# Optimization experiments

Measured on AMD Instinct MI355X. Metric: run time of the kernel, lower is better.

Reference implementation:

```python
import jax, jax.numpy as jnp
import numpy as np

B = 64          # decode batch (one token per sequence)
HID = 4096      # hidden_size
HQ = 32         # num query heads
HKV = 8         # num kv heads (GQA, groups = 4)
D = 128         # head_dim
BS = 16         # block_size of paged KV cache
MAXB = 64       # max blocks per sequence -> max context 1024
MAXPOS = 4096   # rope table length
TOTAL_SLOTS = B * MAXB * BS


def setup_inputs() -> dict:
    key = jax.random.key(0)
    ks = jax.random.split(key, 10)
    hidden = jax.random.normal(ks[0], (B, 1, HID), jnp.float32)
    context_lens = jax.random.randint(ks[1], (B,), 512, BS * MAXB + 1).astype(jnp.int32)
    positions = (context_lens - 1).reshape(B, 1)  # decoding token position
    # each sequence owns a contiguous range of blocks
    block_tables = jnp.arange(B * MAXB, dtype=jnp.int32).reshape(B, MAXB)
    last = context_lens - 1
    slot_mapping = (block_tables[jnp.arange(B), last // BS] * BS + last % BS).astype(jnp.int32)
    inv_freq = 1.0 / (10000.0 ** (jnp.arange(0, D, 2, dtype=jnp.float32) / D))
    freqs = jnp.outer(jnp.arange(MAXPOS, dtype=jnp.float32), inv_freq)  # [MAXPOS, D/2]
    cos, sin = jnp.cos(freqs), jnp.sin(freqs)
    key_cache = jax.random.normal(ks[2], (TOTAL_SLOTS, HKV, D), jnp.float32) * 0.5
    value_cache = jax.random.normal(ks[3], (TOTAL_SLOTS, HKV, D), jnp.float32) * 0.5
    Wq = jax.random.normal(ks[4], (HQ * D, HID), jnp.float32) * 0.02
    Wk = jax.random.normal(ks[5], (HKV * D, HID), jnp.float32) * 0.02
    Wv = jax.random.normal(ks[6], (HKV * D, HID), jnp.float32) * 0.02
    Wo = jax.random.normal(ks[7], (HID, HQ * D), jnp.float32) * 0.02
    return dict(hidden=hidden, positions=positions, cos=cos, sin=sin,
                key_cache=key_cache, value_cache=value_cache,
                slot_mapping=slot_mapping, block_tables=block_tables,
                context_lens=context_lens, Wq=Wq, Wk=Wk, Wv=Wv, Wo=Wo)


def reference(hidden, positions, cos, sin, key_cache, value_cache,
              slot_mapping, block_tables, context_lens, Wq, Wk, Wv, Wo):
    b, s, _ = hidden.shape  # s == 1 (paged decode path)
    q = (hidden @ Wq.T).reshape(b, s, HQ, D)
    k = (hidden @ Wk.T).reshape(b, s, HKV, D)
    v = (hidden @ Wv.T).reshape(b, s, HKV, D)
    # rotary embedding (half-split convention)
    c = cos[positions][:, :, None, :]  # [b,s,1,D/2]
    sn = sin[positions][:, :, None, :]
    def rope(x):
        x1, x2 = jnp.split(x, 2, axis=-1)
        return jnp.concatenate([x1 * c - x2 * sn, x2 * c + x1 * sn], axis=-1)
    q, k = rope(q), rope(k)
    # scatter current token's K/V into the paged cache via slot_mapping
    kc = key_cache.at[slot_mapping].set(k.reshape(-1, HKV, D))
    vc = value_cache.at[slot_mapping].set(v.reshape(-1, HKV, D))
    # gather each sequence's KV via block tables
    T = MAXB * BS
    t = jnp.arange(T)
    slots = block_tables[:, t // BS] * BS + (t % BS)  # [b, T]
    keys = kc[slots]   # [b, T, HKV, D]
    vals = vc[slots]   # [b, T, HKV, D]
    # GQA attention, q has one token per sequence
    G = HQ // HKV
    qg = q.reshape(b, HKV, G, D)
    scores = jnp.einsum('bkgd,btkd->bkgt', qg, keys) / jnp.sqrt(jnp.float32(D))
    mask = t[None, :] < context_lens[:, None]  # [b, T]
    scores = jnp.where(mask[:, None, None, :], scores, -jnp.inf)
    p = jax.nn.softmax(scores, axis=-1)
    out = jnp.einsum('bkgt,btkd->bkgd', p, vals).reshape(b, 1, HQ * D)
    return out @ Wo.T
```

## Files before the change

### kernel.cpp

```cpp
#include <hip/hip_runtime.h>

#define B_    64
#define HID_  4096
#define HQ_   32
#define HKV_  8
#define D_    128
#define BS_   16
#define MAXB_ 64

#define KSPLIT  16
#define KCHUNK  (HID_ / KSPLIT)
#define QKV_ROWS 6144
#define O_ROWS   4096
#define SPLITS  8

#define REGION_SZ ((size_t)KSPLIT * QKV_ROWS * 64)
#define QKVF_SZ  ((size_t)64 * 6144)
#define ATTN_SZ  ((size_t)64 * 4096)
#define XB_SZ    ((size_t)HID_ * 64)

typedef __attribute__((ext_vector_type(8))) short bf16x8;
typedef __attribute__((ext_vector_type(4))) float f32x4;

__device__ inline unsigned short f2bf(float x) {
  union { float f; unsigned u; } v; v.f = x;
  unsigned r = v.u + 0x7fff + ((v.u >> 16) & 1);
  return (unsigned short)(r >> 16);
}
__device__ inline float bf2f(unsigned short h) {
  union { float f; unsigned u; } v; v.u = ((unsigned)h) << 16; return v.f;
}

__global__ __launch_bounds__(256) void convert_x(
    const float* __restrict__ X, unsigned short* __restrict__ XBhi,
    unsigned short* __restrict__ XBlo)
{
  int idx = blockIdx.x * 256 + threadIdx.x;
  int kg = idx >> 6, b = idx & 63;
  const float* xp = X + (size_t)b * HID_ + kg * 8;
  float4 a = *(const float4*)xp, c = *(const float4*)(xp + 4);
  float xs[8] = {a.x, a.y, a.z, a.w, c.x, c.y, c.z, c.w};
  unsigned short hi[8], lo[8];
  #pragma unroll
  for (int j = 0; j < 8; ++j) {
    hi[j] = f2bf(xs[j]);
    lo[j] = f2bf(xs[j] - bf2f(hi[j]));
  }
  *(uint4*)(XBhi + (size_t)idx * 8) = *(const uint4*)hi;
  *(uint4*)(XBlo + (size_t)idx * 8) = *(const uint4*)lo;
}

__global__ __launch_bounds__(256, 4) void gemm_mfma(
    const float* __restrict__ W0, const float* __restrict__ W1,
    const float* __restrict__ W2,
    const unsigned short* __restrict__ XBhi,
    const unsigned short* __restrict__ XBlo,
    int split1, int split2, int rows_total, float* __restrict__ part)
{
  const int tid = threadIdx.x;
  const int l   = tid & 63;
  const int w   = tid >> 6;
  const int r0  = blockIdx.x * 128 + w * 32;
  const int k0  = blockIdx.y * KCHUNK;

  const float* W; int rloc;
  if (r0 < split1)      { W = W0; rloc = r0; }
  else if (r0 < split2) { W = W1; rloc = r0 - split1; }
  else                  { W = W2; rloc = r0 - split2; }

  const int lm = l & 15;
  const int lk = l >> 4;

  const float* wp0 = W + (size_t)(rloc + lm) * HID_ + k0 + lk * 8;
  const float* wp1 = wp0 + (size_t)16 * HID_;
  const unsigned short* bh = XBhi + ((size_t)(k0 / 8 + lk) * 64 + lm) * 8;
  const unsigned short* bl = XBlo + ((size_t)(k0 / 8 + lk) * 64 + lm) * 8;

  f32x4 acc[2][4];
  #pragma unroll
  for (int rt = 0; rt < 2; ++rt)
    #pragma unroll
    for (int ct = 0; ct < 4; ++ct)
      #pragma unroll
      for (int i = 0; i < 4; ++i) acc[rt][ct][i] = 0.f;

  #pragma unroll 2
  for (int ks = 0; ks < KCHUNK / 32; ++ks) {
    bf16x8 Bh[4], Bl[4];
    #pragma unroll
    for (int ct = 0; ct < 4; ++ct) {
      Bh[ct] = *(const bf16x8*)(bh + (size_t)ks * 2048 + ct * 128);
      Bl[ct] = *(const bf16x8*)(bl + (size_t)ks * 2048 + ct * 128);
    }
    #pragma unroll
    for (int rt = 0; rt < 2; ++rt) {
      const float* wp = (rt ? wp1 : wp0) + ks * 32;
      float4 a0 = *(const float4*)wp;
      float4 a1 = *(const float4*)(wp + 4);
      float xs[8] = {a0.x, a0.y, a0.z, a0.w, a1.x, a1.y, a1.z, a1.w};
      bf16x8 Ah, Al;
      #pragma unroll
      for (int j = 0; j < 8; ++j) {
        unsigned short h = f2bf(xs[j]);
        Ah[j] = (short)h;
        Al[j] = (short)f2bf(xs[j] - bf2f(h));
      }
      #pragma unroll
      for (int ct = 0; ct < 4; ++ct) {
        acc[rt][ct] = __builtin_amdgcn_mfma_f32_16x16x32_bf16(Ah, Bh[ct], acc[rt][ct], 0, 0, 0);
        acc[rt][ct] = __builtin_amdgcn_mfma_f32_16x16x32_bf16(Al, Bh[ct], acc[rt][ct], 0, 0, 0);
        acc[rt][ct] = __builtin_amdgcn_mfma_f32_16x16x32_bf16(Ah, Bl[ct], acc[rt][ct], 0, 0, 0);
      }
    }
  }

  #pragma unroll
  for (int rt = 0; rt < 2; ++rt)
    #pragma unroll
    for (int ct = 0; ct < 4; ++ct) {
      int row = r0 + rt * 16 + lk * 4;
      int bat = ct * 16 + lm;
      #pragma unroll
      for (int i = 0; i < 4; ++i)
        part[((size_t)blockIdx.y * rows_total + row + i) * 64 + bat] = acc[rt][ct][i];
    }
}

__global__ __launch_bounds__(256) void reduce_rope(
    const float* __restrict__ part, const float* __restrict__ cosT,
    const float* __restrict__ sinT, const int* __restrict__ positions,
    float* __restrict__ qkvf)
{
  const int bb  = threadIdx.x & 63;
  const int cid = blockIdx.x * 4 + (threadIdx.x >> 6);
  const int pos = positions[bb];

  if (cid < 2048) {
    const int hq = cid >> 6, d0 = cid & 63;
    const int r1 = hq * 128 + d0;
    float x1 = 0.f, x2 = 0.f;
    #pragma unroll 8
    for (int ks = 0; ks < KSPLIT; ++ks) {
      x1 += part[((size_t)ks * QKV_ROWS + r1) * 64 + bb];
      x2 += part[((size_t)ks * QKV_ROWS + r1 + 64) * 64 + bb];
    }
    float c = cosT[pos * 64 + d0], s = sinT[pos * 64 + d0];
    const float scale = 0.08838834764831843f;
    qkvf[(size_t)(bb * 32 + hq) * 128 + d0]      = (x1 * c - x2 * s) * scale;
    qkvf[(size_t)(bb * 32 + hq) * 128 + d0 + 64] = (x2 * c + x1 * s) * scale;
  } else if (cid < 2560) {
    const int c2 = cid - 2048;
    const int kh = c2 >> 6, d0 = c2 & 63;
    const int r1 = 4096 + kh * 128 + d0;
    float x1 = 0.f, x2 = 0.f;
    #pragma unroll 8
    for (int ks = 0; ks < KSPLIT; ++ks) {
      x1 += part[((size_t)ks * QKV_ROWS + r1) * 64 + bb];
      x2 += part[((size_t)ks * QKV_ROWS + r1 + 64) * 64 + bb];
    }
    float c = cosT[pos * 64 + d0], s = sinT[pos * 64 + d0];
    qkvf[262144 + (size_t)(bb * 8 + kh) * 128 + d0]      = x1 * c - x2 * s;
    qkvf[262144 + (size_t)(bb * 8 + kh) * 128 + d0 + 64] = x2 * c + x1 * s;
  } else {
    const int c2 = cid - 2560;
    const int kh = c2 >> 6, d0 = c2 & 63;
    const int r1 = 5120 + kh * 128 + d0;
    float x1 = 0.f, x2 = 0.f;
    #pragma unroll 8
    for (int ks = 0; ks < KSPLIT; ++ks) {
      x1 += part[((size_t)ks * QKV_ROWS + r1) * 64 + bb];
      x2 += part[((size_t)ks * QKV_ROWS + r1 + 64) * 64 + bb];
    }
    qkvf[327680 + (size_t)(bb * 8 + kh) * 128 + d0]      = x1;
    qkvf[327680 + (size_t)(bb * 8 + kh) * 128 + d0 + 64] = x2;
  }
}

__global__ __launch_bounds__(256) void attn_split(
    const float* __restrict__ qkvf, const float* __restrict__ kcache,
    const float* __restrict__ vcache, const int* __restrict__ btab,
    const int* __restrict__ ctxlen,
    float* __restrict__ part_o,
    float* __restrict__ part_ml)
{
  const int bid = blockIdx.x;
  const int s   = bid & (SPLITS - 1);
  const int bh  = bid >> 3;
  const int b = bh >> 3, h = bh & 7;
  const int ctx   = ctxlen[b];
  const int chunk = (ctx + SPLITS - 1) / SPLITS;
  const int t0 = s * chunk;
  const int t1 = min(ctx, t0 + chunk);
  const int n  = t1 - t0;
  const int last = ctx - 1;

  const int tid  = threadIdx.x;
  const int half = tid >> 5;
  const int d4   = tid & 31;

  __shared__ float sc[4][128];
  __shared__ float oacc[8][4][128];
  __shared__ float red[4][2];

  float4 qf[4];
  #pragma unroll
  for (int g = 0; g < 4; ++g)
    qf[g] = *(const float4*)(qkvf + (size_t)(b * 32 + h * 4 + g) * 128 + d4 * 4);

  const float* knew = qkvf + 262144 + (size_t)(b * 8 + h) * 128;
  const float* vnew = qkvf + 327680 + (size_t)(b * 8 + h) * 128;

  for (int t = t0 + half; t < t1; t += 8) {
    const float* kp;
    if (t == last) kp = knew;
    else {
      int slot = btab[b * MAXB_ + (t >> 4)] * BS_ + (t & 15);
      kp = kcache + ((size_t)slot * HKV_ + h) * D_;
    }
    float4 kv = *(const float4*)(kp + d4 * 4);
    float p0 = qf[0].x * kv.x + qf[0].y * kv.y + qf[0].z * kv.z + qf[0].w * kv.w;
    float p1 = qf[1].x * kv.x + qf[1].y * kv.y + qf[1].z * kv.z + qf[1].w * kv.w;
    float p2 = qf[2].x * kv.x + qf[2].y * kv.y + qf[2].z * kv.z + qf[2].w * kv.w;
    float p3 = qf[3].x * kv.x + qf[3].y * kv.y + qf[3].z * kv.z + qf[3].w * kv.w;
    #pragma unroll
    for (int m = 16; m >= 1; m >>= 1) {
      p0 += __shfl_xor(p0, m);
      p1 += __shfl_xor(p1, m);
      p2 += __shfl_xor(p2, m);
      p3 += __shfl_xor(p3, m);
    }
    if (d4 == 0) {
      int i = t - t0;
      sc[0][i] = p0; sc[1][i] = p1; sc[2][i] = p2; sc[3][i] = p3;
    }
  }
  __syncthreads();

  {
    const int w = tid >> 6, l = tid & 63;
    float mx = -1e30f;
    for (int i = l; i < n; i += 64) mx = fmaxf(mx, sc[w][i]);
    #pragma unroll
    for (int m = 32; m >= 1; m >>= 1) mx = fmaxf(mx, __shfl_xor(mx, m));
    float lsum = 0.f;
    for (int i = l; i < n; i += 64) {
      float p = __expf(sc[w][i] - mx);
      sc[w][i] = p;
      lsum += p;
    }
    #pragma unroll
    for (int m = 32; m >= 1; m >>= 1) lsum += __shfl_xor(lsum, m);
    if (l == 0) { red[w][0] = mx; red[w][1] = lsum; }
  }
  __syncthreads();

  float acc[4][4] = {{0.f}};
  for (int t = t0 + half; t < t1; t += 8) {
    const float* vp;
    if (t == last) vp = vnew;
    else {
      int slot = btab[b * MAXB_ + (t >> 4)] * BS_ + (t & 15);
      vp = vcache + ((size_t)slot * HKV_ + h) * D_;
    }
    float4 vv = *(const float4*)(vp + d4 * 4);
    int i = t - t0;
    #pragma unroll
    for (int g = 0; g < 4; ++g) {
      float p = sc[g][i];
      acc[g][0] += p * vv.x; acc[g][1] += p * vv.y;
      acc[g][2] += p * vv.z; acc[g][3] += p * vv.w;
    }
  }
  #pragma unroll
  for (int g = 0; g < 4; ++g)
    #pragma unroll
    for (int j = 0; j < 4; ++j)
      oacc[half][g][d4 * 4 + j] = acc[g][j];
  __syncthreads();

  for (int idx = tid; idx < 512; idx += 256) {
    int g = idx >> 7, d = idx & 127;
    float v = 0.f;
    #pragma unroll
    for (int hh = 0; hh < 8; ++hh) v += oacc[hh][g][d];
    part_o[(size_t)bid * 512 + idx] = v;
  }
  if (tid < 8) part_ml[(size_t)bid * 8 + tid] = red[tid >> 1][tid & 1];
}

__global__ __launch_bounds__(256) void attn_combine(
    const float* __restrict__ part_o, const float* __restrict__ part_ml,
    float* __restrict__ attn_out)
{
  const int bh = blockIdx.x;
  const int tid = threadIdx.x;

  __shared__ float Sg[SPLITS][4];
  __shared__ float Dg[4];

  if (tid < 32) {
    int s = tid >> 2, g = tid & 3;
    float m = part_ml[((size_t)bh * SPLITS + s) * 8 + g * 2];
    float l = part_ml[((size_t)bh * SPLITS + s) * 8 + g * 2 + 1];
    float M = m;
    #pragma unroll
    for (int k = 4; k <= 16; k <<= 1) M = fmaxf(M, __shfl_xor(M, k));
    float scl = __expf(m - M);
    float dl = l * scl;
    #pragma unroll
    for (int k = 4; k <= 16; k <<= 1) dl += __shfl_xor(dl, k);
    Sg[s][g] = scl;
    if (s == 0) Dg[g] = dl;
  }
  __syncthreads();

  for (int idx = tid; idx < 512; idx += 256) {
    int g = idx >> 7;
    float num = 0.f;
    #pragma unroll
    for (int s = 0; s < SPLITS; ++s)
      num += Sg[s][g] * part_o[((size_t)bh * SPLITS + s) * 512 + idx];
    attn_out[(size_t)bh * 512 + idx] = num / Dg[g];
  }
}

__global__ __launch_bounds__(256) void reduce_out_t(
    const float* __restrict__ part, float* __restrict__ out)
{
  __shared__ float t[64][65];
  const int i0 = blockIdx.x * 64;
  const int lane = threadIdx.x & 63, q = threadIdx.x >> 6;

  #pragma unroll
  for (int rr = q; rr < 64; rr += 4) {
    float s = 0.f;
    #pragma unroll 8
    for (int ks = 0; ks < KSPLIT; ++ks)
      s += part[((size_t)ks * O_ROWS + i0 + rr) * 64 + lane];
    t[rr][lane] = s;
  }
  __syncthreads();
  #pragma unroll
  for (int rr = q; rr < 64; rr += 4)
    out[(size_t)rr * O_ROWS + i0 + lane] = t[lane][rr];
}

extern "C" void kernel_launch(void* const* d_in, const int* in_sizes, int n_in,
                              void* d_out, int out_size, void* d_ws, size_t ws_size,
                              hipStream_t stream)
{
  (void)in_sizes; (void)n_in; (void)out_size; (void)ws_size;
  const float* hidden    = (const float*)d_in[0];
  const int*   positions = (const int*)d_in[1];
  const float* cosT      = (const float*)d_in[2];
  const float* sinT      = (const float*)d_in[3];
  const float* kcache    = (const float*)d_in[4];
  const float* vcache    = (const float*)d_in[5];
  const int*   btab      = (const int*)d_in[7];
  const int*   ctx       = (const int*)d_in[8];
  const float* Wq        = (const float*)d_in[9];
  const float* Wk        = (const float*)d_in[10];
  const float* Wv        = (const float*)d_in[11];
  const float* Wo        = (const float*)d_in[12];
  float* out = (float*)d_out;

  float* ws      = (float*)d_ws;
  float* region  = ws;
  float* qkvf    = region + REGION_SZ;
  float* attn_o  = qkvf + QKVF_SZ;
  unsigned short* XBhi = (unsigned short*)(attn_o + ATTN_SZ);
  unsigned short* XBlo = XBhi + XB_SZ;
  float* part1   = region;
  float* part_o  = region;
  float* part_ml = region + (size_t)B_ * HKV_ * SPLITS * 512;
  float* part3   = region;

  convert_x<<<128, 256, 0, stream>>>(hidden, XBhi, XBlo);
  gemm_mfma<<<dim3(QKV_ROWS / 128, KSPLIT), 256, 0, stream>>>(
      Wq, Wk, Wv, XBhi, XBlo, 4096, 5120, QKV_ROWS, part1);
  reduce_rope<<<768, 256, 0, stream>>>(part1, cosT, sinT, positions, qkvf);
  attn_split<<<B_ * HKV_ * SPLITS, 256, 0, stream>>>(
      qkvf, kcache, vcache, btab, ctx, part_o, part_ml);
  attn_combine<<<B_ * HKV_, 256, 0, stream>>>(part_o, part_ml, attn_o);
  convert_x<<<128, 256, 0, stream>>>(attn_o, XBhi, XBlo);
  gemm_mfma<<<dim3(O_ROWS / 128, KSPLIT), 256, 0, stream>>>(
      Wo, Wo, Wo, XBhi, XBlo, O_ROWS, O_ROWS, O_ROWS, part3);
  reduce_out_t<<<O_ROWS / 64, 256, 0, stream>>>(part3, out);
}
```

Baseline: 203.4 us.

## Fuse attention combine with bf16 split conversion, double K-split, shrink attn LDS

The attention-combine kernel now writes the hi/lo bf16 split layout directly, so the separate convert_x launch and the fp32 attention-output buffer are removed. The GEMM K-split is raised from 16 to 32 with a fully unrolled inner loop, which gives the grid more blocks but makes the reduction kernels read twice as many partials. The attn_split kernel does a cross-half shuffle reduction before writing to a smaller shared buffer, and declares a minimum-occupancy launch bound. Together these aim to cut launch overhead and traffic and raise parallelism, at the cost of more partial-sum memory traffic and a larger workspace region.

```diff
diff --git a/kernel.cpp b/kernel.cpp
--- a/kernel.cpp
+++ b/kernel.cpp
@@ -8,15 +8,15 @@
 #define BS_   16
 #define MAXB_ 64
 
-#define KSPLIT  16
-#define KCHUNK  (HID_ / KSPLIT)
+#define KS1     32
+#define KCHUNK  (HID_ / KS1)
+#define NSTEP   (KCHUNK / 32)
 #define QKV_ROWS 6144
 #define O_ROWS   4096
 #define SPLITS  8
 
-#define REGION_SZ ((size_t)KSPLIT * QKV_ROWS * 64)
+#define REGION_SZ ((size_t)KS1 * QKV_ROWS * 64)
 #define QKVF_SZ  ((size_t)64 * 6144)
-#define ATTN_SZ  ((size_t)64 * 4096)
 #define XB_SZ    ((size_t)HID_ * 64)
 
 typedef __attribute__((ext_vector_type(8))) short bf16x8;
@@ -84,8 +84,8 @@
       #pragma unroll
       for (int i = 0; i < 4; ++i) acc[rt][ct][i] = 0.f;
 
-  #pragma unroll 2
-  for (int ks = 0; ks < KCHUNK / 32; ++ks) {
+  #pragma unroll
+  for (int ks = 0; ks < NSTEP; ++ks) {
     bf16x8 Bh[4], Bl[4];
     #pragma unroll
     for (int ct = 0; ct < 4; ++ct) {
@@ -140,7 +140,7 @@
     const int r1 = hq * 128 + d0;
     float x1 = 0.f, x2 = 0.f;
     #pragma unroll 8
-    for (int ks = 0; ks < KSPLIT; ++ks) {
+    for (int ks = 0; ks < KS1; ++ks) {
       x1 += part[((size_t)ks * QKV_ROWS + r1) * 64 + bb];
       x2 += part[((size_t)ks * QKV_ROWS + r1 + 64) * 64 + bb];
     }
@@ -154,7 +154,7 @@
     const int r1 = 4096 + kh * 128 + d0;
     float x1 = 0.f, x2 = 0.f;
     #pragma unroll 8
-    for (int ks = 0; ks < KSPLIT; ++ks) {
+    for (int ks = 0; ks < KS1; ++ks) {
       x1 += part[((size_t)ks * QKV_ROWS + r1) * 64 + bb];
       x2 += part[((size_t)ks * QKV_ROWS + r1 + 64) * 64 + bb];
     }
@@ -167,7 +167,7 @@
     const int r1 = 5120 + kh * 128 + d0;
     float x1 = 0.f, x2 = 0.f;
     #pragma unroll 8
-    for (int ks = 0; ks < KSPLIT; ++ks) {
+    for (int ks = 0; ks < KS1; ++ks) {
       x1 += part[((size_t)ks * QKV_ROWS + r1) * 64 + bb];
       x2 += part[((size_t)ks * QKV_ROWS + r1 + 64) * 64 + bb];
     }
@@ -176,7 +176,7 @@
   }
 }
 
-__global__ __launch_bounds__(256) void attn_split(
+__global__ __launch_bounds__(256, 8) void attn_split(
     const float* __restrict__ qkvf, const float* __restrict__ kcache,
     const float* __restrict__ vcache, const int* __restrict__ btab,
     const int* __restrict__ ctxlen,
@@ -199,7 +199,7 @@
   const int d4   = tid & 31;
 
   __shared__ float sc[4][128];
-  __shared__ float oacc[8][4][128];
+  __shared__ float wred[4][4][128];
   __shared__ float red[4][2];
 
   float4 qf[4];
@@ -275,24 +275,31 @@
   for (int g = 0; g < 4; ++g)
     #pragma unroll
     for (int j = 0; j < 4; ++j)
-      oacc[half][g][d4 * 4 + j] = acc[g][j];
+      acc[g][j] += __shfl_xor(acc[g][j], 32);
+  if ((tid & 32) == 0) {
+    int wv = tid >> 6;
+    #pragma unroll
+    for (int g = 0; g < 4; ++g)
+      #pragma unroll
+      for (int j = 0; j < 4; ++j)
+        wred[wv][g][d4 * 4 + j] = acc[g][j];
+  }
   __syncthreads();
 
   for (int idx = tid; idx < 512; idx += 256) {
     int g = idx >> 7, d = idx & 127;
-    float v = 0.f;
-    #pragma unroll
-    for (int hh = 0; hh < 8; ++hh) v += oacc[hh][g][d];
+    float v = wred[0][g][d] + wred[1][g][d] + wred[2][g][d] + wred[3][g][d];
     part_o[(size_t)bid * 512 + idx] = v;
   }
   if (tid < 8) part_ml[(size_t)bid * 8 + tid] = red[tid >> 1][tid & 1];
 }
 
-__global__ __launch_bounds__(256) void attn_combine(
+__global__ __launch_bounds__(256) void attn_combine_xb(
     const float* __restrict__ part_o, const float* __restrict__ part_ml,
-    float* __restrict__ attn_out)
+    unsigned short* __restrict__ XBhi, unsigned short* __restrict__ XBlo)
 {
   const int bh = blockIdx.x;
+  const int b = bh >> 3, h = bh & 7;
   const int tid = threadIdx.x;
 
   __shared__ float Sg[SPLITS][4];
@@ -315,12 +322,18 @@
   __syncthreads();
 
   for (int idx = tid; idx < 512; idx += 256) {
-    int g = idx >> 7;
+    int g = idx >> 7, d = idx & 127;
     float num = 0.f;
     #pragma unroll
     for (int s = 0; s < SPLITS; ++s)
       num += Sg[s][g] * part_o[((size_t)bh * SPLITS + s) * 512 + idx];
-    attn_out[(size_t)bh * 512 + idx] = num / Dg[g];
+    float val = num / Dg[g];
+    int col = (h * 4 + g) * 128 + d;
+    int kg = col >> 3, j = col & 7;
+    unsigned short hi = f2bf(val);
+    unsigned short lo = f2bf(val - bf2f(hi));
+    XBhi[((size_t)kg * 64 + b) * 8 + j] = hi;
+    XBlo[((size_t)kg * 64 + b) * 8 + j] = lo;
   }
 }
 
@@ -335,7 +348,7 @@
   for (int rr = q; rr < 64; rr += 4) {
     float s = 0.f;
     #pragma unroll 8
-    for (int ks = 0; ks < KSPLIT; ++ks)
+    for (int ks = 0; ks < KS1; ++ks)
       s += part[((size_t)ks * O_ROWS + i0 + rr) * 64 + lane];
     t[rr][lane] = s;
   }
@@ -367,8 +380,7 @@
   float* ws      = (float*)d_ws;
   float* region  = ws;
   float* qkvf    = region + REGION_SZ;
-  float* attn_o  = qkvf + QKVF_SZ;
-  unsigned short* XBhi = (unsigned short*)(attn_o + ATTN_SZ);
+  unsigned short* XBhi = (unsigned short*)(qkvf + QKVF_SZ);
   unsigned short* XBlo = XBhi + XB_SZ;
   float* part1   = region;
   float* part_o  = region;
@@ -376,14 +388,13 @@
   float* part3   = region;
 
   convert_x<<<128, 256, 0, stream>>>(hidden, XBhi, XBlo);
-  gemm_mfma<<<dim3(QKV_ROWS / 128, KSPLIT), 256, 0, stream>>>(
+  gemm_mfma<<<dim3(QKV_ROWS / 128, KS1), 256, 0, stream>>>(
       Wq, Wk, Wv, XBhi, XBlo, 4096, 5120, QKV_ROWS, part1);
   reduce_rope<<<768, 256, 0, stream>>>(part1, cosT, sinT, positions, qkvf);
   attn_split<<<B_ * HKV_ * SPLITS, 256, 0, stream>>>(
       qkvf, kcache, vcache, btab, ctx, part_o, part_ml);
-  attn_combine<<<B_ * HKV_, 256, 0, stream>>>(part_o, part_ml, attn_o);
-  convert_x<<<128, 256, 0, stream>>>(attn_o, XBhi, XBlo);
-  gemm_mfma<<<dim3(O_ROWS / 128, KSPLIT), 256, 0, stream>>>(
+  attn_combine_xb<<<B_ * HKV_, 256, 0, stream>>>(part_o, part_ml, XBhi, XBlo);
+  gemm_mfma<<<dim3(O_ROWS / 128, KS1), 256, 0, stream>>>(
       Wo, Wo, Wo, XBhi, XBlo, O_ROWS, O_ROWS, O_ROWS, part3);
   reduce_out_t<<<O_ROWS / 64, 256, 0, stream>>>(part3, out);
 }
```

Measured after the change: 224.1 us. 1.1x slower.
